# Kernel optimization log

Measured on AMD Instinct MI355X. Metric: run time of the kernel, lower is better.

The kernel has to match this reference:

```python
import jax, jax.numpy as jnp
import numpy as np

B, L, D, H, MD = 8, 1024, 1024, 16, 6
DF = 4 * D
HD = D // H
EPS = 1e-5


def setup_inputs() -> dict:
    key = jax.random.key(0)
    ks = jax.random.split(key, 12)
    s = 0.02
    n = lambda k, shape: jax.random.normal(k, shape, dtype=jnp.float32) * s
    return {
        "x": jax.random.normal(ks[0], (B, L, D), dtype=jnp.float32),
        # attention sub-block
        "attn_norm_w": jnp.ones((D,), jnp.float32),
        "attn_norm_b": jnp.zeros((D,), jnp.float32),
        "in_proj_w": n(ks[1], (3 * D, D)),
        "in_proj_b": jnp.zeros((3 * D,), jnp.float32),
        "out_proj_w": n(ks[2], (D, D)),
        "out_proj_b": jnp.zeros((D,), jnp.float32),
        # ffn sub-block
        "ffn_norm_w": jnp.ones((D,), jnp.float32),
        "ffn_norm_b": jnp.zeros((D,), jnp.float32),
        "ffn_w1": n(ks[3], (DF, D)),
        "ffn_b1": jnp.zeros((DF,), jnp.float32),
        "ffn_w2": n(ks[4], (D, DF)),
        "ffn_b2": jnp.zeros((D,), jnp.float32),
        # router
        "rt_norm_w": jnp.ones((D,), jnp.float32),
        "rt_norm_b": jnp.zeros((D,), jnp.float32),
        "rt_w1": n(ks[5], (D, D)),
        "rt_b1": jnp.zeros((D,), jnp.float32),
        "rt_w2": n(ks[6], (MD, D)),
        "rt_b2": jnp.zeros((MD,), jnp.float32),
    }


def _layernorm(x, w, b):
    mu = jnp.mean(x, axis=-1, keepdims=True)
    var = jnp.mean(jnp.square(x - mu), axis=-1, keepdims=True)
    return (x - mu) * jax.lax.rsqrt(var + EPS) * w + b


def _mha(x, in_proj_w, in_proj_b, out_proj_w, out_proj_b):
    # packed qkv projection, torch nn.MultiheadAttention semantics (batch_first)
    qkv = x @ in_proj_w.T + in_proj_b                      # (B,L,3D)
    q, k, v = jnp.split(qkv, 3, axis=-1)
    def heads(t):
        return t.reshape(B, L, H, HD).transpose(0, 2, 1, 3)  # (B,H,L,HD)
    q, k, v = heads(q), heads(k), heads(v)
    scores = jnp.einsum("bhqd,bhkd->bhqk", q, k) / jnp.sqrt(jnp.float32(HD))
    attn = jax.nn.softmax(scores, axis=-1)
    ctx = jnp.einsum("bhqk,bhkd->bhqd", attn, v)           # (B,H,L,HD)
    ctx = ctx.transpose(0, 2, 1, 3).reshape(B, L, D)
    return ctx @ out_proj_w.T + out_proj_b


def _block(x, p):
    # pre-norm attention + residual
    a_in = _layernorm(x, p["attn_norm_w"], p["attn_norm_b"])
    x = x + _mha(a_in, p["in_proj_w"], p["in_proj_b"], p["out_proj_w"], p["out_proj_b"])
    # pre-norm FFN + residual (exact erf GELU, matching torch nn.GELU default)
    f_in = _layernorm(x, p["ffn_norm_w"], p["ffn_norm_b"])
    h = jax.nn.gelu(f_in @ p["ffn_w1"].T + p["ffn_b1"], approximate=False)
    x = x + h @ p["ffn_w2"].T + p["ffn_b2"]
    return x


def reference(x, attn_norm_w, attn_norm_b, in_proj_w, in_proj_b, out_proj_w,
              out_proj_b, ffn_norm_w, ffn_norm_b, ffn_w1, ffn_b1, ffn_w2,
              ffn_b2, rt_norm_w, rt_norm_b, rt_w1, rt_b1, rt_w2, rt_b2):
    p = dict(attn_norm_w=attn_norm_w, attn_norm_b=attn_norm_b,
             in_proj_w=in_proj_w, in_proj_b=in_proj_b,
             out_proj_w=out_proj_w, out_proj_b=out_proj_b,
             ffn_norm_w=ffn_norm_w, ffn_norm_b=ffn_norm_b,
             ffn_w1=ffn_w1, ffn_b1=ffn_b1, ffn_w2=ffn_w2, ffn_b2=ffn_b2)
    # router (eval mode: argmax, no Gumbel noise)
    r_in = _layernorm(x, rt_norm_w, rt_norm_b)
    h = jax.nn.gelu(r_in @ rt_w1.T + rt_b1, approximate=False)
    logits = h @ rt_w2.T + rt_b2                           # (B,L,MD)
    depths = jnp.argmax(logits, axis=-1) + 1               # (B,L) in [1,MD]
    cur = x
    for level in range(1, MD + 1):
        upd = _block(cur, p)
        cont = (depths >= level)[..., None]
        cur = jnp.where(cont, upd, cur)
    return cur, depths, logits
```

## Files before the change

### kernel.cpp

```cpp
#include <hip/hip_runtime.h>
#include <cstdint>
#include <cstddef>

typedef __bf16 bf16;
typedef bf16 bf16x8 __attribute__((ext_vector_type(8)));
typedef float f32x4 __attribute__((ext_vector_type(4)));

#define GAS __attribute__((address_space(1)))
#define LAS __attribute__((address_space(3)))

__device__ __forceinline__ void async_cp16(const bf16* g, bf16* l) {
  __builtin_amdgcn_global_load_lds((const GAS unsigned int*)g,
                                   (LAS unsigned int*)l, 16, 0, 0);
}

__device__ __forceinline__ float gelu_f(float x) {
  return 0.5f * x * (1.0f + erff(x * 0.70710678118654752440f));
}

__global__ void __launch_bounds__(256) f2b_kernel(const float* __restrict__ in,
                                                  bf16* __restrict__ out, int n) {
  int i = (blockIdx.x * 256 + threadIdx.x) * 4;
  if (i >= n) return;
  float4 v = *(const float4*)&in[i];
  union { uint2 u; bf16 e[4]; } o;
  o.e[0] = (bf16)v.x; o.e[1] = (bf16)v.y; o.e[2] = (bf16)v.z; o.e[3] = (bf16)v.w;
  *(uint2*)&out[i] = o.u;
}

__global__ void __launch_bounds__(256) split3_kernel(const float* __restrict__ in,
    bf16* __restrict__ oh, bf16* __restrict__ om, bf16* __restrict__ ol, int n) {
  int i = (blockIdx.x * 256 + threadIdx.x) * 4;
  if (i >= n) return;
  float4 v = *(const float4*)&in[i];
  float a[4] = {v.x, v.y, v.z, v.w};
  union { uint2 u; bf16 e[4]; } h, m, l;
#pragma unroll
  for (int j = 0; j < 4; j++) {
    h.e[j] = (bf16)a[j];
    float r = a[j] - (float)h.e[j];
    m.e[j] = (bf16)r;
    l.e[j] = (bf16)(r - (float)m.e[j]);
  }
  *(uint2*)&oh[i] = h.u;
  *(uint2*)&om[i] = m.u;
  *(uint2*)&ol[i] = l.u;
}

template<int SPLIT>
__global__ void __launch_bounds__(256) ln_kernel(const float* __restrict__ X,
    const float* __restrict__ w, const float* __restrict__ b,
    bf16* __restrict__ oh, bf16* __restrict__ om, bf16* __restrict__ ol) {
  const int row = blockIdx.x;
  const int tid = threadIdx.x;
  const float4 xv = *(const float4*)&X[(size_t)row * 1024 + tid * 4];
  float s1 = xv.x + xv.y + xv.z + xv.w;
  float s2 = xv.x * xv.x + xv.y * xv.y + xv.z * xv.z + xv.w * xv.w;
#pragma unroll
  for (int d = 1; d < 64; d <<= 1) {
    s1 += __shfl_xor(s1, d, 64);
    s2 += __shfl_xor(s2, d, 64);
  }
  __shared__ float red[8];
  if ((tid & 63) == 0) { red[tid >> 6] = s1; red[4 + (tid >> 6)] = s2; }
  __syncthreads();
  s1 = red[0] + red[1] + red[2] + red[3];
  s2 = red[4] + red[5] + red[6] + red[7];
  const float mu = s1 * (1.0f / 1024.0f);
  const float var = s2 * (1.0f / 1024.0f) - mu * mu;
  const float rs = rsqrtf(var + 1e-5f);
  const float4 wv = *(const float4*)&w[tid * 4];
  const float4 bv = *(const float4*)&b[tid * 4];
  float y[4] = {(xv.x - mu) * rs * wv.x + bv.x,
                (xv.y - mu) * rs * wv.y + bv.y,
                (xv.z - mu) * rs * wv.z + bv.z,
                (xv.w - mu) * rs * wv.w + bv.w};
  union { uint2 u; bf16 e[4]; } h;
#pragma unroll
  for (int j = 0; j < 4; j++) h.e[j] = (bf16)y[j];
  *(uint2*)&oh[(size_t)row * 1024 + tid * 4] = h.u;
  if (SPLIT == 3) {
    union { uint2 u; bf16 e[4]; } m, l;
#pragma unroll
    for (int j = 0; j < 4; j++) {
      float r = y[j] - (float)h.e[j];
      m.e[j] = (bf16)r;
      l.e[j] = (bf16)(r - (float)m.e[j]);
    }
    *(uint2*)&om[(size_t)row * 1024 + tid * 4] = m.u;
    *(uint2*)&ol[(size_t)row * 1024 + tid * 4] = l.u;
  }
}

__global__ void __launch_bounds__(256) ln_c_kernel(const float* __restrict__ X,
    const float* __restrict__ w, const float* __restrict__ b,
    bf16* __restrict__ oh, const int* __restrict__ cnt_ptr) {
  const int row = blockIdx.x;
  const int cnt = *cnt_ptr;
  const int pad = (cnt + 127) & ~127;
  if (row >= pad) return;
  const int tid = threadIdx.x;
  if (row >= cnt) {
    *(uint2*)&oh[(size_t)row * 1024 + tid * 4] = make_uint2(0, 0);
    return;
  }
  const float4 xv = *(const float4*)&X[(size_t)row * 1024 + tid * 4];
  float s1 = xv.x + xv.y + xv.z + xv.w;
  float s2 = xv.x * xv.x + xv.y * xv.y + xv.z * xv.z + xv.w * xv.w;
#pragma unroll
  for (int d = 1; d < 64; d <<= 1) {
    s1 += __shfl_xor(s1, d, 64);
    s2 += __shfl_xor(s2, d, 64);
  }
  __shared__ float red[8];
  if ((tid & 63) == 0) { red[tid >> 6] = s1; red[4 + (tid >> 6)] = s2; }
  __syncthreads();
  s1 = red[0] + red[1] + red[2] + red[3];
  s2 = red[4] + red[5] + red[6] + red[7];
  const float mu = s1 * (1.0f / 1024.0f);
  const float var = s2 * (1.0f / 1024.0f) - mu * mu;
  const float rs = rsqrtf(var + 1e-5f);
  const float4 wv = *(const float4*)&w[tid * 4];
  const float4 bv = *(const float4*)&b[tid * 4];
  union { uint2 u; bf16 e[4]; } h;
  h.e[0] = (bf16)((xv.x - mu) * rs * wv.x + bv.x);
  h.e[1] = (bf16)((xv.y - mu) * rs * wv.y + bv.y);
  h.e[2] = (bf16)((xv.z - mu) * rs * wv.z + bv.z);
  h.e[3] = (bf16)((xv.w - mu) * rs * wv.w + bv.w);
  *(uint2*)&oh[(size_t)row * 1024 + tid * 4] = h.u;
}

__global__ void zero_cnt_kernel(int* cnt_all, int* bcnt_all) {
  if (threadIdx.x < 6) cnt_all[threadIdx.x] = 0;
  if (threadIdx.x < 48) bcnt_all[threadIdx.x] = 0;
}

__global__ void __launch_bounds__(256) build_idx_kernel(
    const int* __restrict__ gate, int* __restrict__ idx_all,
    int* __restrict__ cnt_all, int* __restrict__ bidx_all,
    int* __restrict__ bcnt_all) {
  const int lev = blockIdx.x >> 3;
  const int b   = blockIdx.x & 7;
  const int level = lev + 1;
  int* idx  = idx_all + lev * 8192;
  int* bidx = bidx_all + lev * 8192 + b * 1024;
  for (int t = threadIdx.x; t < 1024; t += 256) {
    const int row = b * 1024 + t;
    if (gate[row] >= level) {
      int p = atomicAdd(&bcnt_all[lev * 8 + b], 1);
      bidx[p] = t;
      int q = atomicAdd(&cnt_all[lev], 1);
      idx[q] = row;
    }
  }
}

__device__ __forceinline__ void swizzle_mn(int gx, int& m0, int& n0) {
  const int id = blockIdx.y * gx + blockIdx.x;
  const int k8 = id & 7, t = id >> 3;
  n0 = (t % gx) * 128;
  m0 = ((t / gx) * 8 + k8) * 128;
}

template<int MODE>
__global__ void __launch_bounds__(256) gemm_nt(
    const bf16* __restrict__ A, const bf16* __restrict__ B,
    const float* __restrict__ bias, const float* __restrict__ Res,
    float* __restrict__ C32, bf16* __restrict__ Cb,
    const int* __restrict__ idx, const int* __restrict__ cnt_ptr,
    int N, int K, int ldc, int coff) {
  __shared__ bf16 As[128 * 32];
  __shared__ bf16 Bs[128 * 32];
  const int tid = threadIdx.x;
  const int w = tid >> 6, lane = tid & 63;
  const int lr = lane & 15, lq = lane >> 4;
  int m0, n0;
  swizzle_mn(gridDim.x, m0, n0);
  int cnt = 0x7fffffff;
  if (MODE != 0) {
    cnt = *cnt_ptr;
    if (m0 >= cnt) return;
  }
  const int wm = (w >> 1) * 64, wn = (w & 1) * 64;

  f32x4 acc[4][4] = {};

  const int i0 = m0 + (tid >> 2), i1 = i0 + 64;
  size_t ar0, ar1;
  if (MODE == 1 || MODE == 2) {
    ar0 = (size_t)idx[i0 < cnt ? i0 : 0];
    ar1 = (size_t)idx[i1 < cnt ? i1 : 0];
  } else {
    ar0 = (size_t)i0; ar1 = (size_t)i1;
  }
  const bf16* ga0 = A + ar0 * K + (tid & 3) * 8;
  const bf16* ga1 = A + ar1 * K + (tid & 3) * 8;
  const bf16* gb = B + (size_t)(n0 + (tid >> 2)) * K + (tid & 3) * 8;
  bf16* la = As + w * 512;
  bf16* lb = Bs + w * 512;
  const size_t bstep = (size_t)64 * K;

  for (int k0 = 0; k0 < K; k0 += 32) {
    __syncthreads();
    async_cp16(ga0 + k0, la);
    async_cp16(ga1 + k0, la + 2048);
    async_cp16(gb + k0, lb);
    async_cp16(gb + bstep + k0, lb + 2048);
    __syncthreads();
    bf16x8 af[4], bfr[4];
#pragma unroll
    for (int i = 0; i < 4; i++)
      af[i] = *(const bf16x8*)&As[(wm + i * 16 + lr) * 32 + lq * 8];
#pragma unroll
    for (int i = 0; i < 4; i++)
      bfr[i] = *(const bf16x8*)&Bs[(wn + i * 16 + lr) * 32 + lq * 8];
#pragma unroll
    for (int mi = 0; mi < 4; mi++)
#pragma unroll
      for (int ni = 0; ni < 4; ni++)
        acc[mi][ni] = __builtin_amdgcn_mfma_f32_16x16x32_bf16(
            af[mi], bfr[ni], acc[mi][ni], 0, 0, 0);
  }

#pragma unroll
  for (int mi = 0; mi < 4; mi++) {
    const int rbase = m0 + wm + mi * 16 + lq * 4;
    int orig[4];
#pragma unroll
    for (int r = 0; r < 4; r++) {
      const int i = rbase + r;
      if (MODE == 1 || MODE == 2 || MODE == 4) orig[r] = (i < cnt) ? idx[i] : -1;
      else orig[r] = i;
    }
#pragma unroll
    for (int ni = 0; ni < 4; ni++) {
      const int c = n0 + wn + ni * 16 + lr;
      const float bv = bias[c];
#pragma unroll
      for (int r = 0; r < 4; r++) {
        const float v = acc[mi][ni][r] + bv;
        const int i = rbase + r;
        if (MODE == 0) {
          Cb[(size_t)i * ldc + coff + c] = (bf16)v;
        } else if (MODE == 1) {
          if (orig[r] >= 0) Cb[(size_t)orig[r] * ldc + c] = (bf16)v;
        } else if (MODE == 2) {
          const float rv = (orig[r] >= 0) ? Res[(size_t)orig[r] * N + c] : 0.0f;
          C32[(size_t)i * N + c] = rv + v;
        } else if (MODE == 3) {
          Cb[(size_t)i * N + c] = (bf16)gelu_f(v);
        } else {
          if (orig[r] >= 0)
            C32[(size_t)orig[r] * N + c] = Res[(size_t)i * N + c] + v;
        }
      }
    }
  }
}

__global__ void __launch_bounds__(256) gemm_router(
    const bf16* __restrict__ Ah, const bf16* __restrict__ Am, const bf16* __restrict__ Al,
    const bf16* __restrict__ Bh, const bf16* __restrict__ Bm, const bf16* __restrict__ Bl,
    float* __restrict__ C32) {
  __shared__ bf16 As[3][128 * 32];
  __shared__ bf16 Bs[3][128 * 32];
  const int tid = threadIdx.x;
  const int w = tid >> 6, lane = tid & 63;
  const int lr = lane & 15, lq = lane >> 4;
  int m0, n0;
  swizzle_mn(gridDim.x, m0, n0);
  const int wm = (w >> 1) * 64, wn = (w & 1) * 64;
  const int K = 1024;

  f32x4 acc[4][4] = {};

  const size_t aoff = (size_t)(m0 + (tid >> 2)) * K + (tid & 3) * 8;
  const size_t boff = (size_t)(n0 + (tid >> 2)) * K + (tid & 3) * 8;
  const bf16* gA[3] = {Ah + aoff, Am + aoff, Al + aoff};
  const bf16* gB[3] = {Bh + boff, Bm + boff, Bl + boff};
  const int lo = w * 512;
  const size_t step64 = (size_t)64 * K;

  const int cA[6] = {0, 0, 1, 1, 0, 2};
  const int cB[6] = {0, 1, 0, 1, 2, 0};

  for (int k0 = 0; k0 < K; k0 += 32) {
    __syncthreads();
#pragma unroll
    for (int j = 0; j < 3; j++) {
      async_cp16(gA[j] + k0, As[j] + lo);
      async_cp16(gA[j] + step64 + k0, As[j] + lo + 2048);
      async_cp16(gB[j] + k0, Bs[j] + lo);
      async_cp16(gB[j] + step64 + k0, Bs[j] + lo + 2048);
    }
    __syncthreads();
#pragma unroll
    for (int c = 0; c < 6; c++) {
      bf16x8 af[4], bfr[4];
#pragma unroll
      for (int i = 0; i < 4; i++)
        af[i] = *(const bf16x8*)&As[cA[c]][(wm + i * 16 + lr) * 32 + lq * 8];
#pragma unroll
      for (int i = 0; i < 4; i++)
        bfr[i] = *(const bf16x8*)&Bs[cB[c]][(wn + i * 16 + lr) * 32 + lq * 8];
#pragma unroll
      for (int mi = 0; mi < 4; mi++)
#pragma unroll
        for (int ni = 0; ni < 4; ni++)
          acc[mi][ni] = __builtin_amdgcn_mfma_f32_16x16x32_bf16(
              af[mi], bfr[ni], acc[mi][ni], 0, 0, 0);
    }
  }

#pragma unroll
  for (int mi = 0; mi < 4; mi++) {
    const int rbase = m0 + wm + mi * 16 + lq * 4;
#pragma unroll
    for (int ni = 0; ni < 4; ni++) {
      const int c = n0 + wn + ni * 16 + lr;
#pragma unroll
      for (int r = 0; r < 4; r++)
        C32[(size_t)(rbase + r) * 1024 + c] = acc[mi][ni][r];
    }
  }
}

__global__ void __launch_bounds__(256) gelu_bias_kernel(float* __restrict__ t,
    const float* __restrict__ bias, int n) {
  int i = (blockIdx.x * 256 + threadIdx.x) * 4;
  if (i >= n) return;
  float4 v = *(const float4*)&t[i];
  float4 bb = *(const float4*)&bias[i & 1023];
  v.x = gelu_f(v.x + bb.x);
  v.y = gelu_f(v.y + bb.y);
  v.z = gelu_f(v.z + bb.z);
  v.w = gelu_f(v.w + bb.w);
  *(float4*)&t[i] = v;
}

__global__ void __launch_bounds__(256) router_logits(const float* __restrict__ h,
    const float* __restrict__ w2, const float* __restrict__ b2,
    float* __restrict__ logits_out, float* __restrict__ depths_out,
    int* __restrict__ gate) {
  const int row = blockIdx.x * 4 + (threadIdx.x >> 6);
  const int lane = threadIdx.x & 63;
  const float* hr = h + (size_t)row * 1024;
  float part[6] = {0, 0, 0, 0, 0, 0};
  for (int kc = lane; kc < 256; kc += 64) {
    float4 hv = *(const float4*)&hr[kc * 4];
#pragma unroll
    for (int j = 0; j < 6; j++) {
      float4 wv = *(const float4*)&w2[j * 1024 + kc * 4];
      part[j] += hv.x * wv.x + hv.y * wv.y + hv.z * wv.z + hv.w * wv.w;
    }
  }
#pragma unroll
  for (int j = 0; j < 6; j++)
#pragma unroll
    for (int d = 1; d < 64; d <<= 1) part[j] += __shfl_xor(part[j], d, 64);
  if (lane == 0) {
    float best = -1e30f;
    int bi = 0;
#pragma unroll
    for (int j = 0; j < 6; j++) {
      const float v = part[j] + b2[j];
      logits_out[(size_t)row * 6 + j] = v;
      if (v > best) { best = v; bi = j; }
    }
    depths_out[row] = (float)(bi + 1);
    gate[row] = bi + 1;
  }
}

__global__ void __launch_bounds__(256) vtrans_kernel(const bf16* __restrict__ qkv,
                                                     bf16* __restrict__ vt) {
  __shared__ bf16 T[64 * 64];
  const int tid = threadIdx.x;
  const int tb = blockIdx.x & 15, bh = blockIdx.x >> 4;
  const int b = bh >> 4, h = bh & 15;
#pragma unroll
  for (int i = 0; i < 2; i++) {
    const int c = tid + i * 256;
    const int tok = c >> 3, hd8 = (c & 7) * 8;
    uint4 v = *(const uint4*)&qkv[((size_t)b * 1024 + tb * 64 + tok) * 3072 + 2048 + h * 64 + hd8];
    *(uint4*)&T[tok * 64 + (hd8 ^ ((tok & 7) << 3))] = v;
  }
  __syncthreads();
#pragma unroll
  for (int i = 0; i < 2; i++) {
    const int c = tid + i * 256;
    const int hd = c >> 3, t8 = (c & 7) * 8;
    union { uint4 u; bf16 e[8]; } o;
#pragma unroll
    for (int j = 0; j < 8; j++)
      o.e[j] = T[(t8 + j) * 64 + (hd ^ (j << 3))];
    *(uint4*)&vt[((size_t)bh * 64 + hd) * 1024 + tb * 64 + t8] = o.u;
  }
}

__global__ void __launch_bounds__(256) attn_kernel(const bf16* __restrict__ qkv,
    const bf16* __restrict__ vtg, bf16* __restrict__ ctx,
    const int* __restrict__ bidx, const int* __restrict__ bcnt) {
  __shared__ bf16 Qs[64 * 72];
  __shared__ bf16 Ks[64 * 72];
  __shared__ bf16 Vt[64 * 72];
  __shared__ bf16 Ps[64 * 72];
  __shared__ int Ts[64];
  const int tid = threadIdx.x;
  const int w = tid >> 6, lane = tid & 63;
  const int lr = lane & 15, lq = lane >> 4;
  const int blk = blockIdx.x;
  const int bh = (blk & 7) | ((blk >> 7) << 3);
  const int qt = (blk >> 3) & 15;
  const int b = bh >> 4, h = bh & 15;
  const int nb = bcnt[b];
  if (qt * 64 >= nb) return;
  const size_t rowbase = (size_t)b * 1024;
  const int hcol = h * 64;
  const size_t vbase = (size_t)bh * 65536;

  if (tid < 64) {
    const int j = qt * 64 + tid;
    Ts[tid] = (j < nb) ? bidx[b * 1024 + j] : bidx[b * 1024 + qt * 64];
  }
  __syncthreads();

#pragma unroll
  for (int i = 0; i < 2; i++) {
    const int c = tid + i * 256;
    const int r = c >> 3, k8 = (c & 7) * 8;
    uint4 v = *(const uint4*)&qkv[(rowbase + Ts[r]) * 3072 + hcol + k8];
    *(uint4*)&Qs[r * 72 + k8] = v;
  }
  __syncthreads();
  bf16x8 aq[2];
#pragma unroll
  for (int hs = 0; hs < 2; hs++)
    aq[hs] = *(const bf16x8*)&Qs[(w * 16 + lr) * 72 + hs * 32 + lq * 8];

  float lsum[4] = {0.0f, 0.0f, 0.0f, 0.0f};
  f32x4 o[4];
#pragma unroll
  for (int i = 0; i < 4; i++) o[i] = (f32x4)0.0f;

  const int Sw = ((w * 4 + lq) & 7) << 3;
  const int Sr = ((w * 4 + (lr >> 2)) & 7) << 3;

  for (int kb = 0; kb < 16; kb++) {
    __syncthreads();
#pragma unroll
    for (int i = 0; i < 2; i++) {
      const int c = tid + i * 256;
      const int r = c >> 3, k8 = (c & 7) * 8;
      uint4 v = *(const uint4*)&qkv[(rowbase + kb * 64 + r) * 3072 + 1024 + hcol + k8];
      *(uint4*)&Ks[r * 72 + k8] = v;
    }
#pragma unroll
    for (int i = 0; i < 2; i++) {
      const int c = tid + i * 256;
      const int hd = c >> 3, t8 = (c & 7) * 8;
      uint4 v = *(const uint4*)&vtg[vbase + (size_t)hd * 1024 + kb * 64 + t8];
      *(uint4*)&Vt[hd * 72 + (t8 ^ (hd & 56))] = v;
    }
    __syncthreads();

    f32x4 s[4];
#pragma unroll
    for (int kf = 0; kf < 4; kf++) {
      f32x4 sa = (f32x4)0.0f;
#pragma unroll
      for (int hs = 0; hs < 2; hs++) {
        bf16x8 bk = *(const bf16x8*)&Ks[(kf * 16 + lr) * 72 + hs * 32 + lq * 8];
        sa = __builtin_amdgcn_mfma_f32_16x16x32_bf16(aq[hs], bk, sa, 0, 0, 0);
      }
      s[kf] = sa;
    }

#pragma unroll
    for (int kf = 0; kf < 4; kf++) {
#pragma unroll
      for (int r = 0; r < 4; r++) {
        const float p = __expf(s[kf][r] * 0.125f);
        lsum[r] += p;
        const int row = w * 16 + lq * 4 + r;
        Ps[row * 72 + ((kf * 16 + lr) ^ Sw)] = (bf16)p;
      }
    }

    bf16x8 ap[2];
#pragma unroll
    for (int ks = 0; ks < 2; ks++)
      ap[ks] = *(const bf16x8*)&Ps[(w * 16 + lr) * 72 + ((ks * 32 + lq * 8) ^ Sr)];
#pragma unroll
    for (int hf = 0; hf < 4; hf++) {
      const int vrow = hf * 16 + lr;
#pragma unroll
      for (int ks = 0; ks < 2; ks++) {
        bf16x8 bv = *(const bf16x8*)&Vt[vrow * 72 + ((ks * 32 + lq * 8) ^ (vrow & 56))];
        o[hf] = __builtin_amdgcn_mfma_f32_16x16x32_bf16(ap[ks], bv, o[hf], 0, 0, 0);
      }
    }
  }

#pragma unroll
  for (int r = 0; r < 4; r++) {
#pragma unroll
    for (int d = 1; d < 16; d <<= 1) lsum[r] += __shfl_xor(lsum[r], d, 64);
  }

#pragma unroll
  for (int r = 0; r < 4; r++) {
    const int rowj = w * 16 + lq * 4 + r;
    if (qt * 64 + rowj < nb) {
      const float inv = 1.0f / lsum[r];
      const size_t row = rowbase + Ts[rowj];
#pragma unroll
      for (int hf = 0; hf < 4; hf++)
        ctx[row * 1024 + hcol + hf * 16 + lr] = (bf16)(o[hf][r] * inv);
    }
  }
}

extern "C" void kernel_launch(void* const* d_in, const int* in_sizes, int n_in,
                              void* d_out, int out_size, void* d_ws, size_t ws_size,
                              hipStream_t stream) {
  (void)in_sizes; (void)n_in; (void)out_size; (void)ws_size;
  const float* x    = (const float*)d_in[0];
  const float* a_nw = (const float*)d_in[1];
  const float* a_nb = (const float*)d_in[2];
  const float* in_w = (const float*)d_in[3];
  const float* in_b = (const float*)d_in[4];
  const float* o_w  = (const float*)d_in[5];
  const float* o_b  = (const float*)d_in[6];
  const float* f_nw = (const float*)d_in[7];
  const float* f_nb = (const float*)d_in[8];
  const float* w1   = (const float*)d_in[9];
  const float* b1   = (const float*)d_in[10];
  const float* w2   = (const float*)d_in[11];
  const float* b2   = (const float*)d_in[12];
  const float* r_nw = (const float*)d_in[13];
  const float* r_nb = (const float*)d_in[14];
  const float* rw1  = (const float*)d_in[15];
  const float* rb1  = (const float*)d_in[16];
  const float* rw2  = (const float*)d_in[17];
  const float* rb2  = (const float*)d_in[18];

  float* cur    = (float*)d_out;
  float* depths = cur + 8388608;
  float* logits = depths + 8192;

  char* ws = (char*)d_ws;
  bf16* wb_in  = (bf16*)(ws + 0);
  bf16* wb_out = (bf16*)(ws + 6291456);
  bf16* wb_f1  = (bf16*)(ws + 8388608);
  bf16* wb_f2  = (bf16*)(ws + 16777216);
  bf16* r1h    = (bf16*)(ws + 25165824);
  bf16* r1m    = (bf16*)(ws + 27262976);
  bf16* r1l    = (bf16*)(ws + 29360128);
  bf16* Abuf   = (bf16*)(ws + 31457280);
  bf16* Bbuf   = (bf16*)(ws + 48234496);
  bf16* Big    = (bf16*)(ws + 65011712);
  float* Tmp   = (float*)(ws + 132120576);
  bf16* VtG    = (bf16*)(ws + 132120576);
  int*  gate   = (int*)(ws + 165675008);
  int* idx_all  = (int*)(ws + 25165824);
  int* bidx_all = (int*)(ws + 27262976);
  int* cnt_all  = (int*)(ws + 29360128);
  int* bcnt_all = cnt_all + 16;

  hipMemcpyAsync(cur, x, (size_t)8388608 * 4, hipMemcpyDeviceToDevice, stream);

  f2b_kernel<<<3072, 256, 0, stream>>>(in_w, wb_in, 3145728);
  f2b_kernel<<<1024, 256, 0, stream>>>(o_w, wb_out, 1048576);
  f2b_kernel<<<4096, 256, 0, stream>>>(w1, wb_f1, 4194304);
  f2b_kernel<<<4096, 256, 0, stream>>>(w2, wb_f2, 4194304);
  split3_kernel<<<1024, 256, 0, stream>>>(rw1, r1h, r1m, r1l, 1048576);

  ln_kernel<3><<<8192, 256, 0, stream>>>(x, r_nw, r_nb, Abuf, Bbuf, Big);
  gemm_router<<<dim3(8, 64), 256, 0, stream>>>(Abuf, Bbuf, Big, r1h, r1m, r1l, Tmp);
  gelu_bias_kernel<<<8192, 256, 0, stream>>>(Tmp, rb1, 8388608);
  router_logits<<<2048, 256, 0, stream>>>(Tmp, rw2, rb2, logits, depths, gate);
  zero_cnt_kernel<<<1, 64, 0, stream>>>(cnt_all, bcnt_all);
  build_idx_kernel<<<48, 256, 0, stream>>>(gate, idx_all, cnt_all, bidx_all, bcnt_all);

  for (int level = 1; level <= 6; level++) {
    const int lev = level - 1;
    const int* idxL  = idx_all + lev * 8192;
    const int* cntL  = cnt_all + lev;
    const int* bidxL = bidx_all + lev * 8192;
    const int* bcntL = bcnt_all + lev * 8;

    ln_kernel<1><<<8192, 256, 0, stream>>>(cur, a_nw, a_nb, Abuf, nullptr, nullptr);
    gemm_nt<0><<<dim3(16, 64), 256, 0, stream>>>(Abuf, wb_in + 1048576, in_b + 1024,
        nullptr, nullptr, Big, nullptr, nullptr, 2048, 1024, 3072, 1024);
    gemm_nt<1><<<dim3(8, 64), 256, 0, stream>>>(Abuf, wb_in, in_b,
        nullptr, nullptr, Big, idxL, cntL, 1024, 1024, 3072, 0);
    vtrans_kernel<<<2048, 256, 0, stream>>>(Big, VtG);
    attn_kernel<<<2048, 256, 0, stream>>>(Big, VtG, Bbuf, bidxL, bcntL);
    gemm_nt<2><<<dim3(8, 64), 256, 0, stream>>>(Bbuf, wb_out, o_b,
        cur, Tmp, nullptr, idxL, cntL, 1024, 1024, 0, 0);
    ln_c_kernel<<<8192, 256, 0, stream>>>(Tmp, f_nw, f_nb, Abuf, cntL);
    gemm_nt<3><<<dim3(32, 64), 256, 0, stream>>>(Abuf, wb_f1, b1,
        nullptr, nullptr, Big, idxL, cntL, 4096, 1024, 0, 0);
    gemm_nt<4><<<dim3(8, 64), 256, 0, stream>>>(Big, wb_f2, b2,
        Tmp, cur, nullptr, idxL, cntL, 1024, 4096, 0, 0);
  }
}
```

Baseline: 2.586 ms.

## Use 3-product router GEMM with 6-product recompute for near-tie rows; BK=64 GEMM

The router GEMM now first runs with only three split-bf16 cross products. Rows whose top-two logits differ by less than 1e-3 are flagged and gathered, then recomputed with all six products, and their logits and argmax are rewritten. Separately, the main gemm_nt doubles its K tile to 64 with XOR-swizzled LDS layouts, which halves barrier count per K. The risk is that the cheaper first pass mis-ranks rows outside the margin, and the extra pass adds launches plus an atomic-built index list.

```diff
diff --git a/kernel.cpp b/kernel.cpp
--- a/kernel.cpp
+++ b/kernel.cpp
@@ -135,6 +135,8 @@
   if (threadIdx.x < 48) bcnt_all[threadIdx.x] = 0;
 }
 
+__global__ void zero_fix_kernel(int* fcnt) { if (threadIdx.x == 0) *fcnt = 0; }
+
 __global__ void __launch_bounds__(256) build_idx_kernel(
     const int* __restrict__ gate, int* __restrict__ idx_all,
     int* __restrict__ cnt_all, int* __restrict__ bidx_all,
@@ -169,8 +171,8 @@
     float* __restrict__ C32, bf16* __restrict__ Cb,
     const int* __restrict__ idx, const int* __restrict__ cnt_ptr,
     int N, int K, int ldc, int coff) {
-  __shared__ bf16 As[128 * 32];
-  __shared__ bf16 Bs[128 * 32];
+  __shared__ bf16 As[128 * 64];
+  __shared__ bf16 Bs[128 * 64];
   const int tid = threadIdx.x;
   const int w = tid >> 6, lane = tid & 63;
   const int lr = lane & 15, lq = lane >> 4;
@@ -185,41 +187,59 @@
 
   f32x4 acc[4][4] = {};
 
-  const int i0 = m0 + (tid >> 2), i1 = i0 + 64;
-  size_t ar0, ar1;
-  if (MODE == 1 || MODE == 2) {
-    ar0 = (size_t)idx[i0 < cnt ? i0 : 0];
-    ar1 = (size_t)idx[i1 < cnt ? i1 : 0];
-  } else {
-    ar0 = (size_t)i0; ar1 = (size_t)i1;
-  }
-  const bf16* ga0 = A + ar0 * K + (tid & 3) * 8;
-  const bf16* ga1 = A + ar1 * K + (tid & 3) * 8;
-  const bf16* gb = B + (size_t)(n0 + (tid >> 2)) * K + (tid & 3) * 8;
-  bf16* la = As + w * 512;
-  bf16* lb = Bs + w * 512;
-  const size_t bstep = (size_t)64 * K;
-
-  for (int k0 = 0; k0 < K; k0 += 32) {
+  const bf16* gA[4];
+  const bf16* gB[4];
+  bf16* lA[4];
+  bf16* lB[4];
+#pragma unroll
+  for (int j = 0; j < 4; j++) {
+    const int c = w * 4 + j, s = c >> 1, h = c & 1;
+    const int rowp = h * 64 + (lane ^ s);
+    int arow;
+    if (MODE == 1 || MODE == 2) {
+      const int i = m0 + rowp;
+      arow = idx[i < cnt ? i : 0];
+    } else {
+      arow = m0 + rowp;
+    }
+    gA[j] = A + (size_t)arow * K + s * 8;
+    gB[j] = B + (size_t)(n0 + rowp) * K + s * 8;
+    lA[j] = As + s * 1024 + h * 512;
+    lB[j] = Bs + s * 1024 + h * 512;
+  }
+
+  int aoff[2], boff[2];
+#pragma unroll
+  for (int ks = 0; ks < 2; ks++) {
+    const int k8 = ks * 4 + lq;
+    aoff[ks] = k8 * 1024 + (wm >> 6) * 512 + (lr ^ k8) * 8;
+    boff[ks] = k8 * 1024 + (wn >> 6) * 512 + (lr ^ k8) * 8;
+  }
+
+  for (int k0 = 0; k0 < K; k0 += 64) {
     __syncthreads();
-    async_cp16(ga0 + k0, la);
-    async_cp16(ga1 + k0, la + 2048);
-    async_cp16(gb + k0, lb);
-    async_cp16(gb + bstep + k0, lb + 2048);
+#pragma unroll
+    for (int j = 0; j < 4; j++) {
+      async_cp16(gA[j], lA[j]);
+      async_cp16(gB[j], lB[j]);
+      gA[j] += 64;
+      gB[j] += 64;
+    }
     __syncthreads();
-    bf16x8 af[4], bfr[4];
-#pragma unroll
-    for (int i = 0; i < 4; i++)
-      af[i] = *(const bf16x8*)&As[(wm + i * 16 + lr) * 32 + lq * 8];
-#pragma unroll
-    for (int i = 0; i < 4; i++)
-      bfr[i] = *(const bf16x8*)&Bs[(wn + i * 16 + lr) * 32 + lq * 8];
-#pragma unroll
-    for (int mi = 0; mi < 4; mi++)
-#pragma unroll
-      for (int ni = 0; ni < 4; ni++)
-        acc[mi][ni] = __builtin_amdgcn_mfma_f32_16x16x32_bf16(
-            af[mi], bfr[ni], acc[mi][ni], 0, 0, 0);
+#pragma unroll
+    for (int ks = 0; ks < 2; ks++) {
+      bf16x8 af[4], bfr[4];
+#pragma unroll
+      for (int i = 0; i < 4; i++) af[i] = *(const bf16x8*)&As[aoff[ks] + i * 128];
+#pragma unroll
+      for (int i = 0; i < 4; i++) bfr[i] = *(const bf16x8*)&Bs[boff[ks] + i * 128];
+#pragma unroll
+      for (int mi = 0; mi < 4; mi++)
+#pragma unroll
+        for (int ni = 0; ni < 4; ni++)
+          acc[mi][ni] = __builtin_amdgcn_mfma_f32_16x16x32_bf16(
+              af[mi], bfr[ni], acc[mi][ni], 0, 0, 0);
+    }
   }
 
 #pragma unroll
@@ -258,44 +278,56 @@
   }
 }
 
+template<int SIX, int GATHER>
 __global__ void __launch_bounds__(256) gemm_router(
     const bf16* __restrict__ Ah, const bf16* __restrict__ Am, const bf16* __restrict__ Al,
     const bf16* __restrict__ Bh, const bf16* __restrict__ Bm, const bf16* __restrict__ Bl,
-    float* __restrict__ C32) {
-  __shared__ bf16 As[3][128 * 32];
-  __shared__ bf16 Bs[3][128 * 32];
+    float* __restrict__ C32, const float* __restrict__ bias,
+    const int* __restrict__ fidx, const int* __restrict__ fcnt_p) {
+  constexpr int SA = SIX ? 3 : 2;
+  __shared__ bf16 As[SA][128 * 32];
+  __shared__ bf16 Bs[SA][128 * 32];
   const int tid = threadIdx.x;
   const int w = tid >> 6, lane = tid & 63;
   const int lr = lane & 15, lq = lane >> 4;
   int m0, n0;
   swizzle_mn(gridDim.x, m0, n0);
+  int fcnt = 0x7fffffff;
+  if (GATHER) {
+    fcnt = *fcnt_p;
+    if (m0 >= fcnt) return;
+  }
   const int wm = (w >> 1) * 64, wn = (w & 1) * 64;
   const int K = 1024;
 
   f32x4 acc[4][4] = {};
 
-  const size_t aoff = (size_t)(m0 + (tid >> 2)) * K + (tid & 3) * 8;
-  const size_t boff = (size_t)(n0 + (tid >> 2)) * K + (tid & 3) * 8;
-  const bf16* gA[3] = {Ah + aoff, Am + aoff, Al + aoff};
-  const bf16* gB[3] = {Bh + boff, Bm + boff, Bl + boff};
+  const int i0 = m0 + (tid >> 2), i1 = i0 + 64;
+  const size_t r0 = GATHER ? (size_t)fidx[i0 < fcnt ? i0 : 0] : (size_t)i0;
+  const size_t r1 = GATHER ? (size_t)fidx[i1 < fcnt ? i1 : 0] : (size_t)i1;
+  const size_t a0 = r0 * K + (tid & 3) * 8, a1 = r1 * K + (tid & 3) * 8;
+  const size_t b0 = (size_t)(n0 + (tid >> 2)) * K + (tid & 3) * 8;
+  const size_t b1o = b0 + (size_t)64 * K;
+  const bf16* tA[3] = {Ah, Am, Al};
+  const bf16* tB[3] = {Bh, Bm, Bl};
   const int lo = w * 512;
-  const size_t step64 = (size_t)64 * K;
 
   const int cA[6] = {0, 0, 1, 1, 0, 2};
   const int cB[6] = {0, 1, 0, 1, 2, 0};
+  constexpr int NP = SIX ? 6 : 3;
 
   for (int k0 = 0; k0 < K; k0 += 32) {
     __syncthreads();
 #pragma unroll
-    for (int j = 0; j < 3; j++) {
-      async_cp16(gA[j] + k0, As[j] + lo);
-      async_cp16(gA[j] + step64 + k0, As[j] + lo + 2048);
-      async_cp16(gB[j] + k0, Bs[j] + lo);
-      async_cp16(gB[j] + step64 + k0, Bs[j] + lo + 2048);
+    for (int t = 0; t < SA; t++) {
+      async_cp16(tA[t] + a0 + k0, As[t] + lo);
+      async_cp16(tA[t] + a1 + k0, As[t] + lo + 2048);
+      async_cp16(tB[t] + b0 + k0, Bs[t] + lo);
+      async_cp16(tB[t] + b1o + k0, Bs[t] + lo + 2048);
     }
     __syncthreads();
 #pragma unroll
-    for (int c = 0; c < 6; c++) {
+    for (int c = 0; c < NP; c++) {
       bf16x8 af[4], bfr[4];
 #pragma unroll
       for (int i = 0; i < 4; i++)
@@ -319,8 +351,15 @@
     for (int ni = 0; ni < 4; ni++) {
       const int c = n0 + wn + ni * 16 + lr;
 #pragma unroll
-      for (int r = 0; r < 4; r++)
-        C32[(size_t)(rbase + r) * 1024 + c] = acc[mi][ni][r];
+      for (int r = 0; r < 4; r++) {
+        const int i = rbase + r;
+        if (GATHER) {
+          if (i < fcnt)
+            C32[(size_t)fidx[i] * 1024 + c] = gelu_f(acc[mi][ni][r] + bias[c]);
+        } else {
+          C32[(size_t)i * 1024 + c] = acc[mi][ni][r];
+        }
+      }
     }
   }
 }
@@ -338,12 +377,15 @@
   *(float4*)&t[i] = v;
 }
 
+template<int FIX>
 __global__ void __launch_bounds__(256) router_logits(const float* __restrict__ h,
     const float* __restrict__ w2, const float* __restrict__ b2,
     float* __restrict__ logits_out, float* __restrict__ depths_out,
-    int* __restrict__ gate) {
+    int* __restrict__ gate, int* __restrict__ flag, int* __restrict__ fidx,
+    int* __restrict__ fcnt) {
   const int row = blockIdx.x * 4 + (threadIdx.x >> 6);
   const int lane = threadIdx.x & 63;
+  if (FIX && !flag[row]) return;
   const float* hr = h + (size_t)row * 1024;
   float part[6] = {0, 0, 0, 0, 0, 0};
   for (int kc = lane; kc < 256; kc += 64) {
@@ -359,16 +401,22 @@
 #pragma unroll
     for (int d = 1; d < 64; d <<= 1) part[j] += __shfl_xor(part[j], d, 64);
   if (lane == 0) {
-    float best = -1e30f;
+    float best = -1e30f, second = -1e30f;
     int bi = 0;
 #pragma unroll
     for (int j = 0; j < 6; j++) {
       const float v = part[j] + b2[j];
       logits_out[(size_t)row * 6 + j] = v;
-      if (v > best) { best = v; bi = j; }
+      if (v > best) { second = best; best = v; bi = j; }
+      else if (v > second) { second = v; }
     }
     depths_out[row] = (float)(bi + 1);
     gate[row] = bi + 1;
+    if (!FIX) {
+      const int fl = (best - second < 1e-3f) ? 1 : 0;
+      flag[row] = fl;
+      if (fl) { int p = atomicAdd(fcnt, 1); fidx[p] = row; }
+    }
   }
 }
 
@@ -562,11 +610,14 @@
   bf16* Big    = (bf16*)(ws + 65011712);
   float* Tmp   = (float*)(ws + 132120576);
   bf16* VtG    = (bf16*)(ws + 132120576);
-  int*  gate   = (int*)(ws + 165675008);
-  int* idx_all  = (int*)(ws + 25165824);
-  int* bidx_all = (int*)(ws + 27262976);
-  int* cnt_all  = (int*)(ws + 29360128);
-  int* bcnt_all = cnt_all + 16;
+  int*  gate     = (int*)(ws + 165675008);
+  int*  flag     = (int*)(ws + 165707776);
+  int*  fidx     = (int*)(ws + 165740544);
+  int*  fcnt     = (int*)(ws + 165773312);
+  int*  idx_all  = (int*)(ws + 165773440);
+  int*  bidx_all = (int*)(ws + 165970048);
+  int*  cnt_all  = (int*)(ws + 166166656);
+  int*  bcnt_all = cnt_all + 16;
 
   hipMemcpyAsync(cur, x, (size_t)8388608 * 4, hipMemcpyDeviceToDevice, stream);
 
@@ -575,11 +626,18 @@
   f2b_kernel<<<4096, 256, 0, stream>>>(w1, wb_f1, 4194304);
   f2b_kernel<<<4096, 256, 0, stream>>>(w2, wb_f2, 4194304);
   split3_kernel<<<1024, 256, 0, stream>>>(rw1, r1h, r1m, r1l, 1048576);
+  zero_fix_kernel<<<1, 64, 0, stream>>>(fcnt);
 
   ln_kernel<3><<<8192, 256, 0, stream>>>(x, r_nw, r_nb, Abuf, Bbuf, Big);
-  gemm_router<<<dim3(8, 64), 256, 0, stream>>>(Abuf, Bbuf, Big, r1h, r1m, r1l, Tmp);
+  gemm_router<0, 0><<<dim3(8, 64), 256, 0, stream>>>(Abuf, Bbuf, Big, r1h, r1m, r1l,
+      Tmp, nullptr, nullptr, nullptr);
   gelu_bias_kernel<<<8192, 256, 0, stream>>>(Tmp, rb1, 8388608);
-  router_logits<<<2048, 256, 0, stream>>>(Tmp, rw2, rb2, logits, depths, gate);
+  router_logits<0><<<2048, 256, 0, stream>>>(Tmp, rw2, rb2, logits, depths, gate,
+      flag, fidx, fcnt);
+  gemm_router<1, 1><<<dim3(8, 64), 256, 0, stream>>>(Abuf, Bbuf, Big, r1h, r1m, r1l,
+      Tmp, rb1, fidx, fcnt);
+  router_logits<1><<<2048, 256, 0, stream>>>(Tmp, rw2, rb2, logits, depths, gate,
+      flag, fidx, fcnt);
   zero_cnt_kernel<<<1, 64, 0, stream>>>(cnt_all, bcnt_all);
   build_idx_kernel<<<48, 256, 0, stream>>>(gate, idx_all, cnt_all, bidx_all, bcnt_all);
 
```

Result: slower. 3.241 ms (+25.3%).
